# Kernel tuning notes

Measured on AMD Instinct MI355X. Metric: run time of the kernel, lower is better.

Reference implementation:

```python
import jax, jax.numpy as jnp
import numpy as np

WINDOW = 16
STRIDE = 8
PADDING = 0
EPS = 1e-6


def setup_inputs() -> dict:
    key = jax.random.key(0)
    x = jax.random.normal(key, (4, 32, 256, 256), dtype=jnp.float32)
    return {"x": x}


def reference(x):
    # Faithful translation of ExtractTensorPatches.forward:
    # grouped conv2d with an (identity + eps) one-hot kernel per channel,
    # so out_i = patch_elem_i + eps * sum(patch).
    B, C, H, W = x.shape
    w2 = WINDOW * WINDOW
    # (w2, 1, w, w): diag = 1+eps, off-diag = eps (matches create_kernel)
    k = (jnp.eye(w2, dtype=x.dtype) + jnp.asarray(EPS, x.dtype)).reshape(
        w2, 1, WINDOW, WINDOW
    )
    k = jnp.tile(k, (C, 1, 1, 1))  # (C*w2, 1, w, w), group-major like torch repeat
    out = jax.lax.conv_general_dilated(
        x,
        k,
        window_strides=(STRIDE, STRIDE),
        padding=[(PADDING, PADDING), (PADDING, PADDING)],
        feature_group_count=C,
        dimension_numbers=("NCHW", "OIHW", "NCHW"),
    )  # (B, C*w2, Ho, Wo)
    Ho, Wo = out.shape[2], out.shape[3]
    out = out.reshape(B, C, WINDOW, WINDOW, Ho * Wo)
    return jnp.transpose(out, (0, 4, 1, 2, 3))  # (B, L, C, w, w)
```

## Files before the change

kernel.cpp:

```cpp
#include <hip/hip_runtime.h>


#define BB   4
#define CC   32
#define HH   256
#define WW   256
#define STR  8
#define HOC  31
#define WOC  31
#define LL   (HOC * WOC)
#define EPSF 1e-6f
#define NXCD 8
#define CGRP 4
#define NGY  (CC / CGRP)

typedef float f4 __attribute__((ext_vector_type(4)));

__global__ __launch_bounds__(256) void
extract_patches_flat(const float* __restrict__ x, float* __restrict__ out) {
    const int nwg  = LL * NGY * BB;
    const int cpx  = nwg / NXCD;
    const int hwid = blockIdx.x + LL * (blockIdx.y + NGY * blockIdx.z);
    const int swz  = (hwid % NXCD) * cpx + (hwid / NXCD);

    const int l    = swz % LL;
    const int rest = swz / LL;
    const int gy   = rest & (NGY - 1);
    const int b    = rest >> 3;

    const int wave = threadIdx.x >> 6;
    const int lane = threadIdx.x & 63;
    const int c    = gy * CGRP + wave;

    const int ho = l / WOC;
    const int wo = l - ho * WOC;
    const int r  = lane >> 2;
    const int q  = lane & 3;

    const float* px = x
        + (((size_t)(b * CC + c) * HH + (size_t)(ho * STR + r)) * WW
           + (size_t)(wo * STR + q * 4));
    const f4 v = *(const f4*)px;

    float s = v.x + v.y + v.z + v.w;
#pragma unroll
    for (int d = 1; d < 64; d <<= 1)
        s += __shfl_xor(s, d, 64);

    const f4 o = v + (EPSF * s);

    float* po = out + (((size_t)b * LL + l) * CC + c) * 256 + (size_t)(lane * 4);
    __builtin_nontemporal_store(o, (f4*)po);
}

extern "C" void kernel_launch(void* const* d_in, const int* in_sizes, int n_in,
                              void* d_out, int out_size, void* d_ws, size_t ws_size,
                              hipStream_t stream) {
    const float* x = (const float*)d_in[0];
    float* out = (float*)d_out;

    dim3 grid(LL, NGY, BB);
    dim3 block(256);
    extract_patches_flat<<<grid, block, 0, stream>>>(x, out);
}
```

Measured before the change: 170.5 us.

## Assign all channels of a patch to one block, eight float4 per thread

Each block now handles one (batch, patch location) pair across all 32 channels, with eight threads per channel each loading eight float4 rows. The full 64-lane shuffle reduction becomes an in-register partial sum followed by a 3-step shuffle, and the grid shrinks by a factor of eight, which cuts launch and reduction overhead. The XCD swizzle is reworked to handle a block count that does not divide evenly. Output stores switch from nontemporal to plain stores, which may change cache pollution behaviour for the large write stream.

```diff
diff --git a/kernel.cpp b/kernel.cpp
--- a/kernel.cpp
+++ b/kernel.cpp
@@ -11,46 +11,52 @@
 #define LL   (HOC * WOC)
 #define EPSF 1e-6f
 #define NXCD 8
-#define CGRP 4
-#define NGY  (CC / CGRP)
 
 typedef float f4 __attribute__((ext_vector_type(4)));
 
 __global__ __launch_bounds__(256) void
-extract_patches_flat(const float* __restrict__ x, float* __restrict__ out) {
-    const int nwg  = LL * NGY * BB;
-    const int cpx  = nwg / NXCD;
-    const int hwid = blockIdx.x + LL * (blockIdx.y + NGY * blockIdx.z);
-    const int swz  = (hwid % NXCD) * cpx + (hwid / NXCD);
-
-    const int l    = swz % LL;
-    const int rest = swz / LL;
-    const int gy   = rest & (NGY - 1);
-    const int b    = rest >> 3;
-
-    const int wave = threadIdx.x >> 6;
-    const int lane = threadIdx.x & 63;
-    const int c    = gy * CGRP + wave;
+extract_patches_fused(const float* __restrict__ x, float* __restrict__ out) {
+    const int nwg  = LL * BB;
+    const int q    = nwg / NXCD;
+    const int rr   = nwg % NXCD;
+    const int hwid = blockIdx.x + LL * blockIdx.y;
+    const int xcd  = hwid & (NXCD - 1);
+    const int idx  = hwid >> 3;
+    const int swz  = (xcd < rr ? xcd * (q + 1)
+                               : rr * (q + 1) + (xcd - rr) * q) + idx;
+    const int l = swz % LL;
+    const int b = swz / LL;
 
     const int ho = l / WOC;
     const int wo = l - ho * WOC;
-    const int r  = lane >> 2;
-    const int q  = lane & 3;
 
-    const float* px = x
-        + (((size_t)(b * CC + c) * HH + (size_t)(ho * STR + r)) * WW
-           + (size_t)(wo * STR + q * 4));
-    const f4 v = *(const f4*)px;
+    const int t   = threadIdx.x;
+    const int c   = t >> 3;
+    const int sub = t & 7;
+    const int r0  = sub >> 2;
+    const int col = (sub & 3) * 4;
 
-    float s = v.x + v.y + v.z + v.w;
+    const float* px = x + ((size_t)(b * CC + c) * HH + (size_t)(ho * STR)) * WW
+                        + (size_t)(wo * STR) + col;
+    f4 v[8];
 #pragma unroll
-    for (int d = 1; d < 64; d <<= 1)
-        s += __shfl_xor(s, d, 64);
+    for (int k = 0; k < 8; ++k)
+        v[k] = *(const f4*)(px + (size_t)(2 * k + r0) * WW);
 
-    const f4 o = v + (EPSF * s);
+    float s = 0.f;
+#pragma unroll
+    for (int k = 0; k < 8; ++k)
+        s += (v[k].x + v[k].y) + (v[k].z + v[k].w);
+    s += __shfl_xor(s, 1, 64);
+    s += __shfl_xor(s, 2, 64);
+    s += __shfl_xor(s, 4, 64);
+    const float e = EPSF * s;
 
-    float* po = out + (((size_t)b * LL + l) * CC + c) * 256 + (size_t)(lane * 4);
-    __builtin_nontemporal_store(o, (f4*)po);
+    float* po = out + ((size_t)b * LL + l) * (CC * 256)
+                    + (size_t)c * 256 + (size_t)(sub * 4);
+#pragma unroll
+    for (int k = 0; k < 8; ++k)
+        *(f4*)(po + k * 32) = v[k] + e;
 }
 
 extern "C" void kernel_launch(void* const* d_in, const int* in_sizes, int n_in,
@@ -59,7 +65,7 @@
     const float* x = (const float*)d_in[0];
     float* out = (float*)d_out;
 
-    dim3 grid(LL, NGY, BB);
+    dim3 grid(LL, BB);
     dim3 block(256);
-    extract_patches_flat<<<grid, block, 0, stream>>>(x, out);
+    extract_patches_fused<<<grid, block, 0, stream>>>(x, out);
 }
```

New measurement: 156.6 us. -8.1%, faster.
